# Performance work log

Measured on AMD Instinct MI355X. Metric: run time of the kernel, lower is better.

Reference implementation:

```python
import jax, jax.numpy as jnp
import numpy as np

# FlowNetC correlation hyperparameters (match init_kwargs)
PAD, K, MD, S1, S2 = 20, 1, 20, 1, 2


def setup_inputs() -> dict:
    key = jax.random.key(0)
    k1, k2 = jax.random.split(key)
    B, C, H, W = 4, 128, 96, 96
    input1 = jax.random.normal(k1, (B, C, H, W), dtype=jnp.float32)
    input2 = jax.random.normal(k2, (B, C, H, W), dtype=jnp.float32)
    return {"input1": input1, "input2": input2}


def _correlation(input1, input2):
    B, C, H, W = input1.shape
    k_eff = max(K, 1)
    kr = (k_eff - 1) // 2          # kernel radius
    border = kr + MD               # border radius in padded coords
    Hp, Wp = H + 2 * PAD, W + 2 * PAD
    outH = (Hp - 2 * border + S1 - 1) // S1
    outW = (Wp - 2 * border + S1 - 1) // S1
    nd = 2 * (MD // S2) + 1        # displacements per axis (21)

    p1 = jnp.pad(input1, ((0, 0), (0, 0), (PAD, PAD), (PAD, PAD)))
    # pad input2 by an extra MD so every shifted slice is in-range
    p2e = jnp.pad(input2, ((0, 0), (0, 0), (PAD + MD, PAD + MD), (PAD + MD, PAD + MD)))

    offs = (jnp.arange(nd) - nd // 2) * S2
    dy, dx = jnp.meshgrid(offs, offs, indexing="ij")
    disps = jnp.stack([dy.ravel(), dx.ravel()], axis=-1)  # [nd*nd, 2]

    sumelems = jnp.asarray(k_eff * k_eff * C, input1.dtype)
    off0 = border - kr  # valid-window-sum output index of center `border`

    def one(d):
        # shifted view of padded input2 aligned with p1
        sh = jax.lax.dynamic_slice(p2e, (0, 0, MD + d[0], MD + d[1]), (B, C, Hp, Wp))
        prod = jnp.sum(p1 * sh, axis=1)  # [B, Hp, Wp]
        if k_eff > 1:
            prod = jax.lax.reduce_window(prod, 0.0, jax.lax.add,
                                         (1, k_eff, k_eff), (1, 1, 1), "VALID")
        return jax.lax.slice(prod,
                             (0, off0, off0),
                             (B, off0 + (outH - 1) * S1 + 1, off0 + (outW - 1) * S1 + 1),
                             (1, S1, S1)) / sumelems

    corr = jax.lax.map(one, disps)           # [nd*nd, B, outH, outW] (sequential: low memory)
    return jnp.transpose(corr, (1, 0, 2, 3))  # [B, nd*nd, outH, outW]


def reference(input1, input2):
    return _correlation(input1, input2)
```

## Files before the change

### kernel.cpp

```cpp
#include <hip/hip_runtime.h>


#define BB 4
#define CC_ALL 128
#define HH 96
#define WW 96
#define ND 21

typedef __attribute__((ext_vector_type(8))) short short8;
typedef __attribute__((ext_vector_type(4))) float floatx4;

__device__ __forceinline__ ushort f2bf(float f) {
    unsigned u = __builtin_bit_cast(unsigned, f);
    return (ushort)((u + 0x7FFFu + ((u >> 16) & 1u)) >> 16);
}

__global__ __launch_bounds__(256)
void transpose_cvt2(const float* __restrict__ in1, const float* __restrict__ in2,
                    ushort* __restrict__ T1, ushort* __restrict__ T2) {
    const int sel = blockIdx.y;
    const float* __restrict__ src = sel ? in2 : in1;
    ushort* __restrict__ dst = sel ? T2 : T1;
    const float mul = sel ? 1.0f : (1.0f / 128.0f);

    int g  = blockIdx.x * 256 + threadIdx.x;
    int t  = g % 24;
    int t1 = g / 24;
    int kq = t1 % 16;
    int t2 = t1 / 16;
    int y  = t2 % 96;
    int b  = t2 / 96;

    const float* s = src + (((b * CC_ALL + kq * 8) * HH + y) * WW) + 4 * t;
    ushort e0[8], e1[8], o0[8], o1[8];
#pragma unroll
    for (int j = 0; j < 8; ++j) {
        float4 f = *(const float4*)(s + j * (HH * WW));
        e0[j] = f2bf(f.x * mul);
        o0[j] = f2bf(f.y * mul);
        e1[j] = f2bf(f.z * mul);
        o1[j] = f2bf(f.w * mul);
    }
    int base = (((b * 96 + y) * 2 + 0) * 16 + kq) * 48 + 2 * t;
    uint4 w;
    ushort* d0 = dst + base * 8;
    w.x = e0[0] | ((unsigned)e0[1] << 16); w.y = e0[2] | ((unsigned)e0[3] << 16);
    w.z = e0[4] | ((unsigned)e0[5] << 16); w.w = e0[6] | ((unsigned)e0[7] << 16);
    *(uint4*)(d0) = w;
    w.x = e1[0] | ((unsigned)e1[1] << 16); w.y = e1[2] | ((unsigned)e1[3] << 16);
    w.z = e1[4] | ((unsigned)e1[5] << 16); w.w = e1[6] | ((unsigned)e1[7] << 16);
    *(uint4*)(d0 + 8) = w;
    ushort* d1 = d0 + 16 * 48 * 8;
    w.x = o0[0] | ((unsigned)o0[1] << 16); w.y = o0[2] | ((unsigned)o0[3] << 16);
    w.z = o0[4] | ((unsigned)o0[5] << 16); w.w = o0[6] | ((unsigned)o0[7] << 16);
    *(uint4*)(d1) = w;
    w.x = o1[0] | ((unsigned)o1[1] << 16); w.y = o1[2] | ((unsigned)o1[3] << 16);
    w.z = o1[4] | ((unsigned)o1[5] << 16); w.w = o1[6] | ((unsigned)o1[7] << 16);
    *(uint4*)(d1 + 8) = w;
}

__global__ __launch_bounds__(256)
void corr_mfma(const ushort* __restrict__ T1, const ushort* __restrict__ T2,
               float* __restrict__ out) {
    __shared__ float lds[4 * ND * 100];

    const int n_   = blockIdx.x;
    const int k    = n_ & 7;
    const int j    = n_ >> 3;
    const int b    = k >> 1;
    const int half = k & 1;
    const int yt   = half * 12 + (j % 12);
    const int dyi  = j / 12;

    const int tid  = threadIdx.x;
    const int w    = tid >> 6;
    const int lane = tid & 63;
    const int nn   = lane & 15;
    const int q    = lane >> 4;
    const int y    = yt * 4 + w;
    const int dy   = 2 * (dyi - 10);
    const int Y2   = y + dy;
    const bool rowok = (unsigned)Y2 < (unsigned)HH;

    const int TS_t[7] = {0, 0, 1, 1, 1, 2, 2};
    const int TS_s[7] = {0, 1, 0, 1, 2, 1, 2};

    floatx4 acc[14];
#pragma unroll
    for (int i = 0; i < 14; ++i) acc[i] = (floatx4)(0.0f);

    const ushort* A0 = T1 + ((b * 96 + y) * 2) * 6144;

    if (rowok) {
        const ushort* B0 = T2 + ((b * 96 + Y2) * 2) * 6144;
#pragma unroll
        for (int ch = 0; ch < 4; ++ch) {
            const int kofs = (4 * ch + q) * 384 + nn * 8;
#pragma unroll
            for (int p = 0; p < 2; ++p) {
                const ushort* Ab = A0 + p * 6144 + kofs;
                const ushort* Bb = B0 + p * 6144 + kofs;
                short8 af0 = *(const short8*)(Ab);
                short8 af1 = *(const short8*)(Ab + 128);
                short8 af2 = *(const short8*)(Ab + 256);
                short8 bf0 = *(const short8*)(Bb);
                short8 bf1 = *(const short8*)(Bb + 128);
                short8 bf2 = *(const short8*)(Bb + 256);
                acc[p*7+0] = __builtin_amdgcn_mfma_f32_16x16x32_bf16(bf0, af0, acc[p*7+0], 0, 0, 0);
                acc[p*7+1] = __builtin_amdgcn_mfma_f32_16x16x32_bf16(bf1, af0, acc[p*7+1], 0, 0, 0);
                acc[p*7+2] = __builtin_amdgcn_mfma_f32_16x16x32_bf16(bf0, af1, acc[p*7+2], 0, 0, 0);
                acc[p*7+3] = __builtin_amdgcn_mfma_f32_16x16x32_bf16(bf1, af1, acc[p*7+3], 0, 0, 0);
                acc[p*7+4] = __builtin_amdgcn_mfma_f32_16x16x32_bf16(bf2, af1, acc[p*7+4], 0, 0, 0);
                acc[p*7+5] = __builtin_amdgcn_mfma_f32_16x16x32_bf16(bf1, af2, acc[p*7+5], 0, 0, 0);
                acc[p*7+6] = __builtin_amdgcn_mfma_f32_16x16x32_bf16(bf2, af2, acc[p*7+6], 0, 0, 0);
            }
        }
    }

    float* wl = lds + w * (ND * 100);
    {
        float4 z = make_float4(0.f, 0.f, 0.f, 0.f);
        for (int kk = lane; kk < (ND * 100) / 4; kk += 64) ((float4*)wl)[kk] = z;
    }
    if (rowok) {
#pragma unroll
        for (int p = 0; p < 2; ++p) {
#pragma unroll
            for (int i = 0; i < 7; ++i) {
                const int t = TS_t[i], s = TS_s[i];
#pragma unroll
                for (int r = 0; r < 4; ++r) {
                    int m = q * 4 + r;
                    int d = 16 * s + m - 16 * t - nn + 10;
                    int x = 2 * (16 * t + nn) + p;
                    if (0 <= d && d <= 20)
                        wl[d * 100 + x] = acc[p * 7 + i][r];
                }
            }
        }
    }
    const int base0 = ((b * (ND * ND) + dyi * ND) * HH + y) * WW;
#pragma unroll
    for (int i = 0; i < 8; ++i) {
        int fl = i * 64 + lane;
        if (fl < 504) {
            int d  = fl / 24;
            int xi = fl % 24;
            float4 v = *(const float4*)(wl + d * 100 + xi * 4);
            *(float4*)(out + base0 + d * (HH * WW) + xi * 4) = v;
        }
    }
}

#define TY 8
#define CCH 4
#define NCHUNK (CC_ALL / CCH)
#define GX 4
#define NTHR 192
#define L1P 52
#define L1U (2 * L1P)
#define W2P 68
#define L2U (2 * W2P)

__global__ __launch_bounds__(NTHR, 2)
void corr_kernel(const float* __restrict__ in1,
                 const float* __restrict__ in2,
                 float* __restrict__ out) {
    __shared__ float lds1[CCH * TY * L1U];
    __shared__ float lds2[CCH * TY * L2U];
    const int tid = threadIdx.x;
    const int y0  = blockIdx.x * TY;
    const int dyi = blockIdx.y;
    const int b   = blockIdx.z;
    const int dy  = 2 * (dyi - 10);
    const int r   = tid / 24;
    const int un_ = tid % 24;
    const int p   = un_ / 12;
    const int u0  = (un_ % 12) * GX;
    float acc[ND * GX];
#pragma unroll
    for (int i = 0; i < ND * GX; ++i) acc[i] = 0.f;
    const float* in1b = in1 + b * (CC_ALL * HH * WW);
    const float* in2b = in2 + b * (CC_ALL * HH * WW);
    {
        float4 z = make_float4(0.f, 0.f, 0.f, 0.f);
        for (int k = tid; k < (CCH * TY * L2U) / 4; k += NTHR)
            ((float4*)lds2)[k] = z;
    }
    for (int ch = 0; ch < NCHUNK; ++ch) {
        const int c0 = ch * CCH;
        __syncthreads();
#pragma unroll
        for (int k = 0; k < 4; ++k) {
            int f  = tid + k * NTHR;
            int x4 = f % 24;
            int rc = f / 24;
            int c  = rc >> 3, rr = rc & 7;
            const float4 g = *(const float4*)&in1b[(c0 + c) * (HH * WW) + (y0 + rr) * WW + x4 * 4];
            float* base = &lds1[(c * TY + rr) * L1U];
            *(float2*)&base[      2 * x4] = make_float2(g.x, g.z);
            *(float2*)&base[L1P + 2 * x4] = make_float2(g.y, g.w);
        }
#pragma unroll
        for (int k = 0; k < 4; ++k) {
            int f  = tid + k * NTHR;
            int x4 = f % 24;
            int rc = f / 24;
            int c  = rc >> 3, rr = rc & 7;
            int Y  = y0 + rr + dy;
            if ((unsigned)Y < HH) {
                const float4 g = *(const float4*)&in2b[(c0 + c) * (HH * WW) + Y * WW + x4 * 4];
                float* base = &lds2[(c * TY + rr) * L2U];
                *(float2*)&base[      2 * x4 + 10] = make_float2(g.x, g.z);
                *(float2*)&base[W2P + 2 * x4 + 10] = make_float2(g.y, g.w);
            }
        }
        __syncthreads();
#pragma unroll
        for (int c = 0; c < CCH; ++c) {
            const float* a4  = &lds1[(c * TY + r) * L1U + p * L1P + u0];
            const float* v24 = &lds2[(c * TY + r) * L2U + p * W2P + u0];
            float4 af = *(const float4*)a4;
            float v[24];
#pragma unroll
            for (int m = 0; m < 24; m += 4) {
                float4 t = *(const float4*)&v24[m];
                v[m] = t.x; v[m + 1] = t.y; v[m + 2] = t.z; v[m + 3] = t.w;
            }
#pragma unroll
            for (int id = 0; id < ND; ++id) {
                acc[id * GX + 0] += af.x * v[id + 0];
                acc[id * GX + 1] += af.y * v[id + 1];
                acc[id * GX + 2] += af.z * v[id + 2];
                acc[id * GX + 3] += af.w * v[id + 3];
            }
        }
    }
    const float scale = 1.0f / 128.0f;
#pragma unroll
    for (int id = 0; id < ND; ++id) {
        int d = dyi * ND + id;
        int base = ((b * (ND * ND) + d) * HH + (y0 + r)) * WW;
#pragma unroll
        for (int j = 0; j < GX; ++j) {
            int x = 2 * (u0 + j) + p;
            out[base + x] = acc[id * GX + j] * scale;
        }
    }
}

extern "C" void kernel_launch(void* const* d_in, const int* in_sizes, int n_in,
                              void* d_out, int out_size, void* d_ws, size_t ws_size,
                              hipStream_t stream) {
    const float* in1 = (const float*)d_in[0];
    const float* in2 = (const float*)d_in[1];
    float* out = (float*)d_out;
    const size_t elems = (size_t)BB * CC_ALL * HH * WW;
    const size_t need  = 2 * elems * sizeof(ushort);

    if (ws_size >= need) {
        ushort* T1 = (ushort*)d_ws;
        ushort* T2 = T1 + elems;
        dim3 tg(147456 / 256, 2);
        hipLaunchKernelGGL(transpose_cvt2, tg, dim3(256), 0, stream, in1, in2, T1, T2);
        hipLaunchKernelGGL(corr_mfma, dim3(2016), dim3(256), 0, stream, T1, T2, out);
    } else {
        dim3 grid(HH / TY, ND, BB);
        hipLaunchKernelGGL(corr_kernel, grid, dim3(NTHR), 0, stream, in1, in2, out);
    }
}
```

Before: 119.3 us.

## Share input1 row across waves via LDS, regroup blocks by displacement rows

Each block now covers one output row and three dy displacements (one per wave) instead of four rows and one dy. The shared input1 row (24KB bf16) is staged once into LDS and reused by all three waves, which cuts redundant global A loads. The grid grows to 2688 blocks of 192 threads. Output stores become nontemporal to avoid cache pollution. The cost is an extra LDS copy plus two barriers per block, and fewer threads per block.

```diff
diff --git a/kernel.cpp b/kernel.cpp
--- a/kernel.cpp
+++ b/kernel.cpp
@@ -59,46 +59,55 @@
     *(uint4*)(d1 + 8) = w;
 }
 
-__global__ __launch_bounds__(256)
+__global__ __launch_bounds__(192)
 void corr_mfma(const ushort* __restrict__ T1, const ushort* __restrict__ T2,
                float* __restrict__ out) {
-    __shared__ float lds[4 * ND * 100];
+    __shared__ __align__(16) float lds[3 * ND * 100];
 
     const int n_   = blockIdx.x;
     const int k    = n_ & 7;
     const int j    = n_ >> 3;
     const int b    = k >> 1;
     const int half = k & 1;
-    const int yt   = half * 12 + (j % 12);
-    const int dyi  = j / 12;
+    const int y    = half * 48 + (j % 48);
+    const int g    = j / 48;
 
     const int tid  = threadIdx.x;
     const int w    = tid >> 6;
     const int lane = tid & 63;
     const int nn   = lane & 15;
     const int q    = lane >> 4;
-    const int y    = yt * 4 + w;
+    const int dyi  = g * 3 + w;
     const int dy   = 2 * (dyi - 10);
     const int Y2   = y + dy;
     const bool rowok = (unsigned)Y2 < (unsigned)HH;
 
+    {
+        const float4* __restrict__ srcA =
+            (const float4*)(T1 + ((b * 96 + y) * 2) * 6144);
+        float4* dstA = (float4*)lds;
+#pragma unroll
+        for (int i = 0; i < 8; ++i)
+            dstA[tid + i * 192] = srcA[tid + i * 192];
+    }
+    __syncthreads();
+
     const int TS_t[7] = {0, 0, 1, 1, 1, 2, 2};
     const int TS_s[7] = {0, 1, 0, 1, 2, 1, 2};
 
     floatx4 acc[14];
 #pragma unroll
-    for (int i = 0; i < 14; ++i) acc[i] = (floatx4)(0.0f);
-
-    const ushort* A0 = T1 + ((b * 96 + y) * 2) * 6144;
+    for (int i = 0; i < 14; ++i) acc[i] = (floatx4){0.f, 0.f, 0.f, 0.f};
 
     if (rowok) {
+        const ushort* Alds = (const ushort*)lds;
         const ushort* B0 = T2 + ((b * 96 + Y2) * 2) * 6144;
 #pragma unroll
         for (int ch = 0; ch < 4; ++ch) {
             const int kofs = (4 * ch + q) * 384 + nn * 8;
 #pragma unroll
             for (int p = 0; p < 2; ++p) {
-                const ushort* Ab = A0 + p * 6144 + kofs;
+                const ushort* Ab = Alds + p * 6144 + kofs;
                 const ushort* Bb = B0 + p * 6144 + kofs;
                 short8 af0 = *(const short8*)(Ab);
                 short8 af1 = *(const short8*)(Ab + 128);
@@ -116,11 +125,12 @@
             }
         }
     }
+    __syncthreads();
 
     float* wl = lds + w * (ND * 100);
     {
-        float4 z = make_float4(0.f, 0.f, 0.f, 0.f);
-        for (int kk = lane; kk < (ND * 100) / 4; kk += 64) ((float4*)wl)[kk] = z;
+        floatx4 z = {0.f, 0.f, 0.f, 0.f};
+        for (int kk = lane; kk < (ND * 100) / 4; kk += 64) ((floatx4*)wl)[kk] = z;
     }
     if (rowok) {
 #pragma unroll
@@ -146,8 +156,8 @@
         if (fl < 504) {
             int d  = fl / 24;
             int xi = fl % 24;
-            float4 v = *(const float4*)(wl + d * 100 + xi * 4);
-            *(float4*)(out + base0 + d * (HH * WW) + xi * 4) = v;
+            floatx4 v = *(const floatx4*)(wl + d * 100 + xi * 4);
+            __builtin_nontemporal_store(v, (floatx4*)(out + base0 + d * (HH * WW) + xi * 4));
         }
     }
 }
@@ -242,9 +252,9 @@
         int d = dyi * ND + id;
         int base = ((b * (ND * ND) + d) * HH + (y0 + r)) * WW;
 #pragma unroll
-        for (int j = 0; j < GX; ++j) {
-            int x = 2 * (u0 + j) + p;
-            out[base + x] = acc[id * GX + j] * scale;
+        for (int jj = 0; jj < GX; ++jj) {
+            int x = 2 * (u0 + jj) + p;
+            out[base + x] = acc[id * GX + jj] * scale;
         }
     }
 }
@@ -263,7 +273,7 @@
         ushort* T2 = T1 + elems;
         dim3 tg(147456 / 256, 2);
         hipLaunchKernelGGL(transpose_cvt2, tg, dim3(256), 0, stream, in1, in2, T1, T2);
-        hipLaunchKernelGGL(corr_mfma, dim3(2016), dim3(256), 0, stream, T1, T2, out);
+        hipLaunchKernelGGL(corr_mfma, dim3(2688), dim3(192), 0, stream, T1, T2, out);
     } else {
         dim3 grid(HH / TY, ND, BB);
         hipLaunchKernelGGL(corr_kernel, grid, dim3(NTHR), 0, stream, in1, in2, out);
```

New measurement: 111.0 us, median of 2. 7.0% less time.
